# Optimization experiments

Measured on AMD Instinct MI355X. Metric: run time of the kernel, lower is better.

Reference implementation:

```python
import jax, jax.numpy as jnp
import numpy as np

HIDDEN = 2048
INTER = 8192
COMPRESSION = 128.9

def _n_ctrl(out_size, in_size):
    return max(16, int(out_size * in_size / COMPRESSION))

def _catmull_rom_grid(n_ctrl, n_samples):
    # static (numpy, float64) sampling grid over [0, n_ctrl-1] to avoid fp32 precision loss
    t = np.linspace(0.0, n_ctrl - 1.0, n_samples, dtype=np.float64)
    i = np.clip(np.floor(t).astype(np.int64), 0, n_ctrl - 2)
    f = (t - i).astype(np.float32)
    idx = np.stack([np.clip(i + k, 0, n_ctrl - 1) for k in (-1, 0, 1, 2)], axis=0)  # [4, N]
    return jnp.asarray(idx.astype(np.int32)), jnp.asarray(f)

def spline_reconstruct(control_points, out_size, in_size):
    """Cubic (Catmull-Rom, order-3) interpolation of 1D control points to a dense [out,in] weight."""
    n = out_size * in_size
    idx, f = _catmull_rom_grid(control_points.shape[0], n)
    p0, p1, p2, p3 = control_points[idx[0]], control_points[idx[1]], control_points[idx[2]], control_points[idx[3]]
    f2 = f * f
    f3 = f2 * f
    w = 0.5 * (2.0 * p1 + (p2 - p0) * f
               + (2.0 * p0 - 5.0 * p1 + 4.0 * p2 - p3) * f2
               + (3.0 * p1 - p0 - 3.0 * p2 + p3) * f3)
    return w.reshape(out_size, in_size)

def setup_inputs() -> dict:
    key = jax.random.key(0)
    k0, k1, k2, k3 = jax.random.split(key, 4)
    hidden_states = jax.random.normal(k0, (4, 2048, HIDDEN), dtype=jnp.float32)
    gate_cp = jax.random.normal(k1, (_n_ctrl(INTER, HIDDEN),), dtype=jnp.float32) * 0.02
    up_cp = jax.random.normal(k2, (_n_ctrl(INTER, HIDDEN),), dtype=jnp.float32) * 0.02
    down_cp = jax.random.normal(k3, (_n_ctrl(HIDDEN, INTER),), dtype=jnp.float32) * 0.02
    return {"hidden_states": hidden_states, "gate_cp": gate_cp, "up_cp": up_cp, "down_cp": down_cp}

def reference(hidden_states, gate_cp, up_cp, down_cp):
    gate_w = spline_reconstruct(gate_cp, INTER, HIDDEN)   # [I, H]
    up_w = spline_reconstruct(up_cp, INTER, HIDDEN)       # [I, H]
    down_w = spline_reconstruct(down_cp, HIDDEN, INTER)   # [H, I]
    gate = jnp.einsum('bsh,ih->bsi', hidden_states, gate_w)
    up = jnp.einsum('bsh,ih->bsi', hidden_states, up_w)
    inter = jax.nn.silu(gate) * up
    return jnp.einsum('bsi,hi->bsh', inter, down_w)
```

## Files before the change

### kernel.cpp

```cpp
#include <hip/hip_runtime.h>
#include <hip/hip_bf16.h>
#include <math.h>

using bf16 = __hip_bfloat16;
typedef __bf16 bf16x8 __attribute__((ext_vector_type(8)));
typedef float  f32x4  __attribute__((ext_vector_type(4)));

#define BK 64

__global__ void spline_recon8_kernel(const float* __restrict__ cp,
                                     bf16* __restrict__ w,
                                     int n8, int n_ctrl, double step) {
    int k8 = blockIdx.x * blockDim.x + threadIdx.x;
    if (k8 >= n8) return;
    long long kbase = (long long)k8 * 8;
    bf16x8 o;
#pragma unroll
    for (int u = 0; u < 8; ++u) {
        double t = (double)(kbase + u) * step;
        int i = (int)t;
        if (i > n_ctrl - 2) i = n_ctrl - 2;
        float f = (float)(t - (double)i);
        float p0 = cp[i > 0 ? i - 1 : 0];
        float p1 = cp[i];
        float p2 = cp[i + 1];
        float p3 = cp[(i + 2) <= (n_ctrl - 1) ? (i + 2) : (n_ctrl - 1)];
        float f2 = f * f;
        float f3 = f2 * f;
        float v = 0.5f * (2.0f * p1
                          + (p2 - p0) * f
                          + (2.0f * p0 - 5.0f * p1 + 4.0f * p2 - p3) * f2
                          + (3.0f * p1 - p0 - 3.0f * p2 + p3) * f3);
        o[u] = (__bf16)v;
    }
    *reinterpret_cast<bf16x8*>(w + kbase) = o;
}

__global__ void cvt_f32_bf16_8_kernel(const float4* __restrict__ x,
                                      bf16* __restrict__ y, int n8) {
    int k = blockIdx.x * blockDim.x + threadIdx.x;
    if (k >= n8) return;
    float4 a = x[2 * k];
    float4 b = x[2 * k + 1];
    bf16x8 o;
    o[0] = (__bf16)a.x; o[1] = (__bf16)a.y; o[2] = (__bf16)a.z; o[3] = (__bf16)a.w;
    o[4] = (__bf16)b.x; o[5] = (__bf16)b.y; o[6] = (__bf16)b.z; o[7] = (__bf16)b.w;
    *reinterpret_cast<bf16x8*>(y + (long long)k * 8) = o;
}

__device__ __forceinline__ void async_load16(const bf16* g, bf16* l) {
    __builtin_amdgcn_global_load_lds(
        (const __attribute__((address_space(1))) void*)g,
        (__attribute__((address_space(3))) void*)l,
        16, 0, 0);
}

__device__ __forceinline__ void raw_barrier() {
    asm volatile("" ::: "memory");
    __builtin_amdgcn_s_barrier();
    asm volatile("" ::: "memory");
}

__global__ __launch_bounds__(512, 4) void fused_gate_up_kernel(
    const bf16* __restrict__ A,
    const bf16* __restrict__ Bg,
    const bf16* __restrict__ Bu,
    bf16* __restrict__ C,
    int M, int N, int K) {
    __shared__ __align__(16) bf16 smem[3 * 128 * BK];
    bf16* As  = smem;
    bf16* Bgs = smem + 128 * BK;
    bf16* Bus = smem + 2 * 128 * BK;

    const int tid  = threadIdx.x;
    const int lane = tid & 63;
    const int wave = tid >> 6;
    const int wq   = wave & 3;
    const int wm   = (wq >> 1) * 64;
    const int wn   = (wq & 1) * 64;
    const bool is_gate = wave < 4;

    const long long brow = (long long)blockIdx.y * 128;
    const long long bcol = (long long)blockIdx.x * 128;

    const int srow = tid >> 3;
    const int skb  = ((tid & 7) ^ (srow & 7)) * 8;
    const bf16* ga0 = A  + (brow + srow) * (long long)K + skb;
    const bf16* ga1 = A  + (brow + srow + 64) * (long long)K + skb;
    const bf16* gg0 = Bg + (bcol + srow) * (long long)K + skb;
    const bf16* gg1 = Bg + (bcol + srow + 64) * (long long)K + skb;
    const bf16* gu0 = Bu + (bcol + srow) * (long long)K + skb;
    const bf16* gu1 = Bu + (bcol + srow + 64) * (long long)K + skb;
    bf16* la0 = As  + tid * 8;
    bf16* la1 = As  + 4096 + tid * 8;
    bf16* lg0 = Bgs + tid * 8;
    bf16* lg1 = Bgs + 4096 + tid * 8;
    bf16* lu0 = Bus + tid * 8;
    bf16* lu1 = Bus + 4096 + tid * 8;

    const bf16* Bsel = is_gate ? Bgs : Bus;
    const int fm = wm + (lane & 15);
    const int fn = wn + (lane & 15);
    const int qk = lane >> 4;

    f32x4 acc[4][4] = {};

    for (int k0 = 0; k0 < K; k0 += BK) {
        async_load16(ga0, la0); ga0 += BK;
        async_load16(ga1, la1); ga1 += BK;
        async_load16(gg0, lg0); gg0 += BK;
        async_load16(gg1, lg1); gg1 += BK;
        async_load16(gu0, lu0); gu0 += BK;
        async_load16(gu1, lu1); gu1 += BK;
        __syncthreads();

#pragma unroll
        for (int h = 0; h < 2; ++h) {
            bf16x8 afr[4], bfr[4];
            const int hc = (h << 2) | qk;
            const int ccA = (hc ^ (fm & 7)) * 8;
            const int ccB = (hc ^ (fn & 7)) * 8;
#pragma unroll
            for (int i = 0; i < 4; ++i)
                afr[i] = *reinterpret_cast<const bf16x8*>(
                    &As[(fm + i * 16) * BK + ccA]);
#pragma unroll
            for (int j = 0; j < 4; ++j)
                bfr[j] = *reinterpret_cast<const bf16x8*>(
                    &Bsel[(fn + j * 16) * BK + ccB]);
#pragma unroll
            for (int i = 0; i < 4; ++i)
#pragma unroll
                for (int j = 0; j < 4; ++j)
                    acc[i][j] = __builtin_amdgcn_mfma_f32_16x16x32_bf16(
                        afr[i], bfr[j], acc[i][j], 0, 0, 0);
        }
        __syncthreads();
    }

    bf16* Epi = smem;
    if (is_gate) {
#pragma unroll
        for (int i = 0; i < 4; ++i)
#pragma unroll
            for (int j = 0; j < 4; ++j)
#pragma unroll
                for (int r = 0; r < 4; ++r) {
                    int row = wm + i * 16 + (lane >> 4) * 4 + r;
                    int col = wn + j * 16 + (lane & 15);
                    float v = acc[i][j][r];
                    float s = v / (1.0f + expf(-v));
                    Epi[row * 128 + col] = __float2bfloat16(s);
                }
    }
    __syncthreads();
    if (!is_gate) {
#pragma unroll
        for (int i = 0; i < 4; ++i)
#pragma unroll
            for (int j = 0; j < 4; ++j)
#pragma unroll
                for (int r = 0; r < 4; ++r) {
                    int row = wm + i * 16 + (lane >> 4) * 4 + r;
                    int col = wn + j * 16 + (lane & 15);
                    float s = __bfloat162float(Epi[row * 128 + col]);
                    float v = s * acc[i][j][r];
                    C[(brow + row) * (long long)N + bcol + col] = __float2bfloat16(v);
                }
    }
}

__global__ __launch_bounds__(512, 2) void gemm_down6_kernel(
    const bf16* __restrict__ A,
    const bf16* __restrict__ B,
    float* __restrict__ C,
    int M, int N, int K) {
    __shared__ __align__(16) bf16 smem[2 * 3 * 128 * BK];
    bf16* As0 = smem;
    bf16* Bs0 = smem + 128 * BK;
    bf16* As1 = smem + 3 * 128 * BK;
    bf16* Bs1 = smem + 4 * 128 * BK;

    const int tid  = threadIdx.x;
    const int lane = tid & 63;
    const int wave = tid >> 6;
    const int wm   = (wave >> 2) * 64;
    const int wn   = (wave & 3) * 64;

    const int b = blockIdx.x;
    const long long brow = (long long)((b & 7) * 8 + (b >> 6)) * 128;
    const long long bcol = (long long)((b >> 3) & 7) * 256;

    const int srow = tid >> 3;
    const int skb  = ((tid & 7) ^ (srow & 7)) * 8;
    const bf16* ga0 = A + (brow + srow) * (long long)K + skb;
    const bf16* ga1 = A + (brow + srow + 64) * (long long)K + skb;
    const bf16* gb0 = B + (bcol + srow) * (long long)K + skb;
    const bf16* gb1 = B + (bcol + srow + 64) * (long long)K + skb;
    const bf16* gb2 = B + (bcol + srow + 128) * (long long)K + skb;
    const bf16* gb3 = B + (bcol + srow + 192) * (long long)K + skb;

    const int fm = wm + (lane & 15);
    const int fn = wn + (lane & 15);
    const int qk = lane >> 4;

    f32x4 acc[4][4] = {};

#define STAGE_DOWN(dA, dB, t)                                              \
    do {                                                                   \
        long long off = (long long)(t) * BK;                               \
        async_load16(ga0 + off, (dA) + tid * 8);                           \
        async_load16(ga1 + off, (dA) + 4096 + tid * 8);                    \
        async_load16(gb0 + off, (dB) + tid * 8);                           \
        async_load16(gb1 + off, (dB) + 4096 + tid * 8);                    \
        async_load16(gb2 + off, (dB) + 8192 + tid * 8);                    \
        async_load16(gb3 + off, (dB) + 12288 + tid * 8);                   \
    } while (0)

#define COMPUTE_DOWN(sA, sB)                                               \
    do {                                                                   \
        _Pragma("unroll")                                                  \
        for (int h = 0; h < 2; ++h) {                                      \
            bf16x8 afr[4], bfr[4];                                         \
            const int hc = (h << 2) | qk;                                  \
            const int ccA = (hc ^ (fm & 7)) * 8;                           \
            const int ccB = (hc ^ (fn & 7)) * 8;                           \
            _Pragma("unroll")                                              \
            for (int i = 0; i < 4; ++i)                                    \
                afr[i] = *reinterpret_cast<const bf16x8*>(                 \
                    &(sA)[(fm + i * 16) * BK + ccA]);                      \
            _Pragma("unroll")                                              \
            for (int j = 0; j < 4; ++j)                                    \
                bfr[j] = *reinterpret_cast<const bf16x8*>(                 \
                    &(sB)[(fn + j * 16) * BK + ccB]);                      \
            _Pragma("unroll")                                              \
            for (int i = 0; i < 4; ++i)                                    \
                _Pragma("unroll")                                          \
                for (int j = 0; j < 4; ++j)                                \
                    acc[i][j] = __builtin_amdgcn_mfma_f32_16x16x32_bf16(   \
                        afr[i], bfr[j], acc[i][j], 0, 0, 0);               \
        }                                                                  \
    } while (0)

#define WAIT_VM6() asm volatile("s_waitcnt vmcnt(6)" ::: "memory")
#define WAIT_VM0() asm volatile("s_waitcnt vmcnt(0)" ::: "memory")

    const int nt = K / BK;

    STAGE_DOWN(As0, Bs0, 0);
    STAGE_DOWN(As1, Bs1, 1);
    WAIT_VM6();
    raw_barrier();

    for (int t = 0; t + 2 < nt; t += 2) {
        COMPUTE_DOWN(As0, Bs0);
        raw_barrier();
        STAGE_DOWN(As0, Bs0, t + 2);
        WAIT_VM6();
        raw_barrier();
        COMPUTE_DOWN(As1, Bs1);
        raw_barrier();
        STAGE_DOWN(As1, Bs1, t + 3);
        WAIT_VM6();
        raw_barrier();
    }
    COMPUTE_DOWN(As0, Bs0);
    WAIT_VM0();
    raw_barrier();
    COMPUTE_DOWN(As1, Bs1);
#undef STAGE_DOWN
#undef COMPUTE_DOWN
#undef WAIT_VM6
#undef WAIT_VM0

#pragma unroll
    for (int i = 0; i < 4; ++i)
#pragma unroll
        for (int j = 0; j < 4; ++j)
#pragma unroll
            for (int r = 0; r < 4; ++r) {
                long long row = brow + wm + i * 16 + qk * 4 + r;
                long long col = bcol + wn + j * 16 + (lane & 15);
                C[row * N + col] = acc[i][j][r];
            }
}

extern "C" void kernel_launch(void* const* d_in, const int* in_sizes, int n_in,
                              void* d_out, int out_size, void* d_ws, size_t ws_size,
                              hipStream_t stream) {
    const float* hs  = (const float*)d_in[0];
    const float* gcp = (const float*)d_in[1];
    const float* ucp = (const float*)d_in[2];
    const float* dcp = (const float*)d_in[3];

    const int M = 8192;
    const int H = 2048;
    const int I = 8192;
    const int NW = H * I;
    const int n_ctrl_g = in_sizes[1];
    const int n_ctrl_u = in_sizes[2];
    const int n_ctrl_d = in_sizes[3];

    bf16* Xb    = (bf16*)d_ws;
    bf16* Wg    = Xb + (size_t)M * H;
    bf16* Wu    = Wg + (size_t)NW;
    bf16* Wd    = Wu + (size_t)NW;
    bf16* inter = Wd + (size_t)NW;

    const int nX8 = (M * H) / 8;
    cvt_f32_bf16_8_kernel<<<(nX8 + 255) / 256, 256, 0, stream>>>(
        (const float4*)hs, Xb, nX8);

    double step_g = (double)(n_ctrl_g - 1) / (double)(NW - 1);
    double step_u = (double)(n_ctrl_u - 1) / (double)(NW - 1);
    double step_d = (double)(n_ctrl_d - 1) / (double)(NW - 1);
    const int n8 = NW / 8;
    spline_recon8_kernel<<<(n8 + 255) / 256, 256, 0, stream>>>(gcp, Wg, n8, n_ctrl_g, step_g);
    spline_recon8_kernel<<<(n8 + 255) / 256, 256, 0, stream>>>(ucp, Wu, n8, n_ctrl_u, step_u);
    spline_recon8_kernel<<<(n8 + 255) / 256, 256, 0, stream>>>(dcp, Wd, n8, n_ctrl_d, step_d);

    fused_gate_up_kernel<<<dim3(I / 128, M / 128), 512, 0, stream>>>(
        Xb, Wg, Wu, inter, M, I, H);

    gemm_down6_kernel<<<512, 512, 0, stream>>>(
        inter, Wd, (float*)d_out, M, H, I);
}
```

Measured before the change: 890.7 us.

## Double-buffer LDS in fused gate/up GEMM with async prefetch pipeline

Replaces the single-buffered gate/up GEMM main loop with a two-stage LDS ping-pong. Loads for the next K tile are issued asynchronously while the current tile is computed, using vmcnt waits and raw barriers, matching the pattern already used in the down kernel. This doubles LDS use to 96KB and lowers the launch bounds occupancy hint from 4 to 2 blocks, trading occupancy for overlap of global loads with MFMA work.

```diff
diff --git a/kernel.cpp b/kernel.cpp
--- a/kernel.cpp
+++ b/kernel.cpp
@@ -61,16 +61,22 @@
     asm volatile("" ::: "memory");
 }
 
-__global__ __launch_bounds__(512, 4) void fused_gate_up_kernel(
+#define WAIT_VM6() asm volatile("s_waitcnt vmcnt(6)" ::: "memory")
+#define WAIT_VM0() asm volatile("s_waitcnt vmcnt(0)" ::: "memory")
+
+__global__ __launch_bounds__(512, 2) void fused_gate_up_kernel(
     const bf16* __restrict__ A,
     const bf16* __restrict__ Bg,
     const bf16* __restrict__ Bu,
     bf16* __restrict__ C,
     int M, int N, int K) {
-    __shared__ __align__(16) bf16 smem[3 * 128 * BK];
-    bf16* As  = smem;
-    bf16* Bgs = smem + 128 * BK;
-    bf16* Bus = smem + 2 * 128 * BK;
+    __shared__ __align__(16) bf16 smem[2 * 3 * 128 * BK];
+    bf16* As0  = smem;
+    bf16* Bgs0 = smem + 8192;
+    bf16* Bus0 = smem + 16384;
+    bf16* As1  = smem + 24576;
+    bf16* Bgs1 = smem + 32768;
+    bf16* Bus1 = smem + 40960;
 
     const int tid  = threadIdx.x;
     const int lane = tid & 63;
@@ -91,52 +97,75 @@
     const bf16* gg1 = Bg + (bcol + srow + 64) * (long long)K + skb;
     const bf16* gu0 = Bu + (bcol + srow) * (long long)K + skb;
     const bf16* gu1 = Bu + (bcol + srow + 64) * (long long)K + skb;
-    bf16* la0 = As  + tid * 8;
-    bf16* la1 = As  + 4096 + tid * 8;
-    bf16* lg0 = Bgs + tid * 8;
-    bf16* lg1 = Bgs + 4096 + tid * 8;
-    bf16* lu0 = Bus + tid * 8;
-    bf16* lu1 = Bus + 4096 + tid * 8;
-
-    const bf16* Bsel = is_gate ? Bgs : Bus;
+
     const int fm = wm + (lane & 15);
     const int fn = wn + (lane & 15);
     const int qk = lane >> 4;
 
     f32x4 acc[4][4] = {};
 
-    for (int k0 = 0; k0 < K; k0 += BK) {
-        async_load16(ga0, la0); ga0 += BK;
-        async_load16(ga1, la1); ga1 += BK;
-        async_load16(gg0, lg0); gg0 += BK;
-        async_load16(gg1, lg1); gg1 += BK;
-        async_load16(gu0, lu0); gu0 += BK;
-        async_load16(gu1, lu1); gu1 += BK;
-        __syncthreads();
-
-#pragma unroll
-        for (int h = 0; h < 2; ++h) {
-            bf16x8 afr[4], bfr[4];
-            const int hc = (h << 2) | qk;
-            const int ccA = (hc ^ (fm & 7)) * 8;
-            const int ccB = (hc ^ (fn & 7)) * 8;
-#pragma unroll
-            for (int i = 0; i < 4; ++i)
-                afr[i] = *reinterpret_cast<const bf16x8*>(
-                    &As[(fm + i * 16) * BK + ccA]);
-#pragma unroll
-            for (int j = 0; j < 4; ++j)
-                bfr[j] = *reinterpret_cast<const bf16x8*>(
-                    &Bsel[(fn + j * 16) * BK + ccB]);
-#pragma unroll
-            for (int i = 0; i < 4; ++i)
-#pragma unroll
-                for (int j = 0; j < 4; ++j)
-                    acc[i][j] = __builtin_amdgcn_mfma_f32_16x16x32_bf16(
-                        afr[i], bfr[j], acc[i][j], 0, 0, 0);
-        }
-        __syncthreads();
-    }
+#define STAGE_F(dA, dG, dU, t)                                             \
+    do {                                                                   \
+        long long off = (long long)(t) * BK;                               \
+        async_load16(ga0 + off, (dA) + tid * 8);                           \
+        async_load16(ga1 + off, (dA) + 4096 + tid * 8);                    \
+        async_load16(gg0 + off, (dG) + tid * 8);                           \
+        async_load16(gg1 + off, (dG) + 4096 + tid * 8);                    \
+        async_load16(gu0 + off, (dU) + tid * 8);                           \
+        async_load16(gu1 + off, (dU) + 4096 + tid * 8);                    \
+    } while (0)
+
+#define COMPUTE_F(sA, sG, sU)                                              \
+    do {                                                                   \
+        const bf16* sB = is_gate ? (sG) : (sU);                            \
+        _Pragma("unroll")                                                  \
+        for (int h = 0; h < 2; ++h) {                                      \
+            bf16x8 afr[4], bfr[4];                                         \
+            const int hc = (h << 2) | qk;                                  \
+            const int ccA = (hc ^ (fm & 7)) * 8;                           \
+            const int ccB = (hc ^ (fn & 7)) * 8;                           \
+            _Pragma("unroll")                                              \
+            for (int i = 0; i < 4; ++i)                                    \
+                afr[i] = *reinterpret_cast<const bf16x8*>(                 \
+                    &(sA)[(fm + i * 16) * BK + ccA]);                      \
+            _Pragma("unroll")                                              \
+            for (int j = 0; j < 4; ++j)                                    \
+                bfr[j] = *reinterpret_cast<const bf16x8*>(                 \
+                    &sB[(fn + j * 16) * BK + ccB]);                        \
+            _Pragma("unroll")                                              \
+            for (int i = 0; i < 4; ++i)                                    \
+                _Pragma("unroll")                                          \
+                for (int j = 0; j < 4; ++j)                                \
+                    acc[i][j] = __builtin_amdgcn_mfma_f32_16x16x32_bf16(   \
+                        afr[i], bfr[j], acc[i][j], 0, 0, 0);               \
+        }                                                                  \
+    } while (0)
+
+    const int nt = K / BK;
+
+    STAGE_F(As0, Bgs0, Bus0, 0);
+    STAGE_F(As1, Bgs1, Bus1, 1);
+    WAIT_VM6();
+    raw_barrier();
+
+    for (int t = 0; t + 2 < nt; t += 2) {
+        COMPUTE_F(As0, Bgs0, Bus0);
+        raw_barrier();
+        STAGE_F(As0, Bgs0, Bus0, t + 2);
+        WAIT_VM6();
+        raw_barrier();
+        COMPUTE_F(As1, Bgs1, Bus1);
+        raw_barrier();
+        STAGE_F(As1, Bgs1, Bus1, t + 3);
+        WAIT_VM6();
+        raw_barrier();
+    }
+    COMPUTE_F(As0, Bgs0, Bus0);
+    WAIT_VM0();
+    raw_barrier();
+    COMPUTE_F(As1, Bgs1, Bus1);
+#undef STAGE_F
+#undef COMPUTE_F
 
     bf16* Epi = smem;
     if (is_gate) {
@@ -242,9 +271,6 @@
         }                                                                  \
     } while (0)
 
-#define WAIT_VM6() asm volatile("s_waitcnt vmcnt(6)" ::: "memory")
-#define WAIT_VM0() asm volatile("s_waitcnt vmcnt(0)" ::: "memory")
-
     const int nt = K / BK;
 
     STAGE_DOWN(As0, Bs0, 0);
@@ -270,8 +296,6 @@
     COMPUTE_DOWN(As1, Bs1);
 #undef STAGE_DOWN
 #undef COMPUTE_DOWN
-#undef WAIT_VM6
-#undef WAIT_VM0
 
 #pragma unroll
     for (int i = 0; i < 4; ++i)
```

New measurement: 952.4 us. 6.9% more time.
